# Kernel optimization log

Hardware: AMD Instinct MI355X
Metric: run time of the kernel (lower is better)

The kernel has to match this reference:

```python
import jax, jax.numpy as jnp
import numpy as np

N_QUBITS = 10
N_LAYERS = 4
OUTPUT = 16
BATCH = 4096
DIM = 2 ** N_QUBITS  # 1024, amplitude-embedding dimension


def setup_inputs() -> dict:
    key = jax.random.key(0)
    k1, k2, k3, k4 = jax.random.split(key, 4)
    X = jax.random.normal(k1, (BATCH, DIM), jnp.float32)
    weights = jax.random.normal(k2, (N_LAYERS, N_QUBITS, 3), jnp.float32)  # StronglyEntanglingLayers params
    W = jax.random.normal(k3, (OUTPUT, N_QUBITS), jnp.float32) / np.sqrt(N_QUBITS)
    b = jax.random.normal(k4, (OUTPUT,), jnp.float32) * 0.01
    return {"X": X, "weights": weights, "W": W, "b": b}


def _rot_matrix(phi, theta, omega):
    # PennyLane Rot(phi, theta, omega) = RZ(omega) @ RY(theta) @ RZ(phi)
    c = jnp.cos(theta / 2).astype(jnp.complex64)
    s = jnp.sin(theta / 2).astype(jnp.complex64)
    a = jnp.exp(-0.5j * (phi + omega)) * c
    bq = -jnp.exp(0.5j * (phi - omega)) * s
    cq = jnp.exp(-0.5j * (phi - omega)) * s
    d = jnp.exp(0.5j * (phi + omega)) * c
    return jnp.stack([jnp.stack([a, bq]), jnp.stack([cq, d])])  # (2,2) complex64


def _apply_1q(state, U, q, n):
    # wire 0 is the most-significant bit (PennyLane default.qubit convention)
    A, B = 2 ** q, 2 ** (n - q - 1)
    s = state.reshape(-1, A, 2, B)
    s = jnp.einsum('ij,bajc->baic', U, s)
    return s.reshape(-1, 2 ** n)


def _cnot(state, c, t, n):
    hi, lo = (c, t) if c < t else (t, c)
    s = state.reshape(-1, 2 ** hi, 2, 2 ** (lo - hi - 1), 2, 2 ** (n - lo - 1))
    if c < t:
        # control axis 2, target axis 4
        s0 = s[:, :, 0]                      # (B, H, M, 2, L)
        s1 = jnp.flip(s[:, :, 1], axis=3)    # flip target where control=1
        s = jnp.stack([s0, s1], axis=2)
    else:
        # control axis 4, target axis 2
        s0 = s[:, :, :, :, 0, :]             # (B, H, 2, M, L)
        s1 = jnp.flip(s[:, :, :, :, 1, :], axis=2)
        s = jnp.stack([s0, s1], axis=4)
    return s.reshape(-1, 2 ** n)


def _circuit(X, weights):
    n = N_QUBITS
    # AmplitudeEmbedding (pad_with=0.0; here input dim == 2**n so just normalize)
    nrm = jnp.linalg.norm(X, axis=-1, keepdims=True)
    state = (X / nrm).astype(jnp.complex64)  # (B, 2**n)
    for l in range(N_LAYERS):
        for q in range(n):
            U = _rot_matrix(weights[l, q, 0], weights[l, q, 1], weights[l, q, 2])
            state = _apply_1q(state, U, q, n)
        r = (l % (n - 1)) + 1  # StronglyEntanglingLayers default imprimitive range
        for q in range(n):
            state = _cnot(state, q, (q + r) % n, n)
    probs = state.real ** 2 + state.imag ** 2  # (B, 2**n)
    # <Z_i> = sum_s probs[s] * (1 - 2*bit_i(s)); wire 0 = MSB
    idx = np.arange(2 ** n)
    bits = (idx[:, None] >> np.arange(n - 1, -1, -1)[None, :]) & 1  # (2**n, n)
    signs = jnp.asarray(1 - 2 * bits, jnp.float32)
    return probs @ signs  # (B, n)


def reference(X, weights, W, b):
    z = _circuit(X, weights)          # (B, n_qubits)
    return z @ W.T + b                # Linear head; nn.Tanh is defined but unused in forward
```

## Files before the change

kernel.cpp:

```cpp
#include <hip/hip_runtime.h>
#include <stdint.h>

#define NQ 10
#define DIMQ 1024
#define BATCH 4096

typedef float f32x2 __attribute__((ext_vector_type(2)));

#if __has_builtin(__builtin_amdgcn_permlane16_swap)
#define HAS_PL16 1
#else
#define HAS_PL16 0
#endif

__host__ __device__ constexpr int cperm_c(int x, int r) {
  for (int q = 0; q < NQ; ++q) {
    const int c = 9 - q;
    int t = c - r; if (t < 0) t += NQ;
    x ^= ((x >> c) & 1) << t;
  }
  return x;
}
constexpr int amask(int q) {
  int a = 0;
  for (int b = 0; b < 6; ++b) a |= ((cperm_c(1 << b, 4) >> (9 - q)) & 1) << b;
  return a;
}
constexpr int mmask(int q) {
  int m = 0;
  for (int b = 0; b < 4; ++b) m |= ((cperm_c(1 << (6 + b), 4) >> (9 - q)) & 1) << b;
  return m;
}

__global__ __launch_bounds__(256) void prep_g(const float* __restrict__ wts,
                                              float* __restrict__ Gg) {
  const int idx = blockIdx.x * 256 + threadIdx.x;
  if (idx < 40) {
    float th = wts[idx * 3 + 1];
    ((float2*)Gg)[idx] = make_float2(cosf(0.5f * th), sinf(0.5f * th));
  }
  f32x2* D0 = (f32x2*)(Gg + 128);
  f32x2* E  = D0 + 1024;
  auto sphase = [&](int l, int i, int comp) {
    float s = 0.f;
    #pragma unroll
    for (int q = 0; q < 10; ++q) {
      float sg = ((i >> (9 - q)) & 1) ? 0.5f : -0.5f;
      s += sg * wts[(l * 10 + q) * 3 + comp];
    }
    return s;
  };
  float p0 = sphase(0, idx, 0);
  D0[idx] = (f32x2){cosf(p0), sinf(p0)};
  #pragma unroll
  for (int l = 0; l < 3; ++l) {
    float a = sphase(l, idx, 2) + sphase(l + 1, cperm_c(idx, l + 1), 0);
    E[l * 1024 + idx] = (f32x2){cosf(a), sinf(a)};
  }
}

template<int CTRL>
__device__ __forceinline__ float dpp1(float x) {
  return __int_as_float(
      __builtin_amdgcn_update_dpp(0, __float_as_int(x), CTRL, 0xF, 0xF, true));
}
template<int P>
__device__ __forceinline__ float shufl(float x) {
  if constexpr (P == 0)      return dpp1<0xB1>(x);
  else if constexpr (P == 1) return dpp1<0x4E>(x);
  else if constexpr (P == 2) return dpp1<0x141>(dpp1<0x1B>(x));
  else                       return dpp1<0x128>(x);
}
__device__ __forceinline__ float x16(float x, bool hi) {
#if HAS_PL16
  auto rr = __builtin_amdgcn_permlane16_swap(__float_as_uint(x),
                                             __float_as_uint(x), false, false);
  return __uint_as_float(hi ? rr[0] : rr[1]);
#else
  (void)hi;
  return __int_as_float(__builtin_amdgcn_ds_swizzle(__float_as_int(x), 0x401F));
#endif
}

__device__ __forceinline__ float red64(float v) {
  v += dpp1<0xB1>(v);
  v += dpp1<0x4E>(v);
  v += dpp1<0x141>(dpp1<0x1B>(v));
  v += dpp1<0x128>(v);
#if HAS_PL16
  { auto rr = __builtin_amdgcn_permlane16_swap(__float_as_uint(v),
                                               __float_as_uint(v), false, false);
    v = __uint_as_float(rr[0]) + __uint_as_float(rr[1]); }
#else
  v += __int_as_float(__builtin_amdgcn_ds_swizzle(__float_as_int(v), 0x401F));
#endif
  auto p = __builtin_amdgcn_permlane32_swap(__float_as_uint(v),
                                            __float_as_uint(v), false, false);
  return __uint_as_float(p[0]) + __uint_as_float(p[1]);
}

template<int MT>
__device__ __forceinline__ void ry_reg(f32x2 (&s)[16], float2 cs) {
  const float c = cs.x, sn = cs.y;
  #pragma unroll
  for (int e0 = 0; e0 < 16; ++e0) {
    if (e0 & MT) continue;
    const int e1 = e0 | MT;
    f32x2 x0 = s[e0], x1 = s[e1];
    s[e0] = c * x0 - sn * x1;
    s[e1] = sn * x0 + c * x1;
  }
}
template<int P>
__device__ __forceinline__ void ry_dpp(f32x2 (&s)[16], float2 cs, int lane) {
  const float c = cs.x;
  const float ss = ((lane >> P) & 1) ? cs.y : -cs.y;
  #pragma unroll
  for (int e = 0; e < 16; ++e) {
    f32x2 o;
    o.x = shufl<P>(s[e].x);
    o.y = shufl<P>(s[e].y);
    s[e] = c * s[e] + ss * o;
  }
}
__device__ __forceinline__ void ry16(f32x2 (&s)[16], float2 cs, int lane) {
  const bool H = (lane & 16) != 0;
  const float c = cs.x;
  const float ss = H ? cs.y : -cs.y;
  #pragma unroll
  for (int e = 0; e < 16; ++e) {
    f32x2 o;
    o.x = x16(s[e].x, H);
    o.y = x16(s[e].y, H);
    s[e] = c * s[e] + ss * o;
  }
}
__device__ __forceinline__ void ry5(f32x2 (&s)[16], float2 cs, int lane) {
  const int L = lane >> 5;
  const float c = cs.x;
  const float ss = L ? cs.y : -cs.y;
  #pragma unroll
  for (int e = 0; e < 16; ++e) {
    unsigned xr = __float_as_uint(s[e].x), xi = __float_as_uint(s[e].y);
    auto rr = __builtin_amdgcn_permlane32_swap(xr, xr, false, false);
    auto ri = __builtin_amdgcn_permlane32_swap(xi, xi, false, false);
    f32x2 o;
    o.x = __uint_as_float(L ? rr[0] : rr[1]);
    o.y = __uint_as_float(L ? ri[0] : ri[1]);
    s[e] = c * s[e] + ss * o;
  }
}

template<int R>
__device__ __forceinline__ void perm_state(f32x2 (&s)[16], f32x2* __restrict__ L,
                                           int lane) {
  constexpr int K0=cperm_c(1,R),  K1=cperm_c(2,R),  K2=cperm_c(4,R),
                K3=cperm_c(8,R),  K4=cperm_c(16,R), K5=cperm_c(32,R),
                C6=cperm_c(64,R), C7=cperm_c(128,R),
                C8=cperm_c(256,R),C9=cperm_c(512,R);
  const int yl = ((lane & 1)  ? K0 : 0) ^ ((lane & 2)  ? K1 : 0) ^
                 ((lane & 4)  ? K2 : 0) ^ ((lane & 8)  ? K3 : 0) ^
                 ((lane & 16) ? K4 : 0) ^ ((lane & 32) ? K5 : 0);
  #pragma unroll
  for (int e = 0; e < 16; ++e) {
    const int ye = ((e & 1) ? C6 : 0) ^ ((e & 2) ? C7 : 0) ^
                   ((e & 4) ? C8 : 0) ^ ((e & 8) ? C9 : 0);
    L[yl ^ ye] = s[e];
  }
  #pragma unroll
  for (int e = 0; e < 16; ++e) s[e] = L[(e << 6) | lane];
}

template<int LYR>
__device__ __forceinline__ void do_layer(f32x2 (&s)[16],
                                         const float2* __restrict__ ryc,
                                         const f32x2* __restrict__ Etab,
                                         f32x2* __restrict__ L, int lane) {
  f32x2 et[16];
  if constexpr (LYR < 3) {
    const f32x2* El = Etab + LYR * 1024;
    #pragma unroll
    for (int e = 0; e < 16; ++e) et[e] = El[(e << 6) | lane];
  }
  const float2* G = ryc + LYR * 10;
  ry_reg<8>(s, G[0]);
  ry_reg<4>(s, G[1]);
  ry_reg<2>(s, G[2]);
  ry_reg<1>(s, G[3]);
  ry5     (s, G[4], lane);
  ry16    (s, G[5], lane);
  ry_dpp<3>(s, G[6], lane);
  ry_dpp<2>(s, G[7], lane);
  ry_dpp<1>(s, G[8], lane);
  ry_dpp<0>(s, G[9], lane);
  if constexpr (LYR < 3) {
    #pragma unroll
    for (int e = 0; e < 16; ++e) {
      f32x2 t = et[e];
      f32x2 r;
      r.x = s[e].x * t.x - s[e].y * t.y;
      r.y = s[e].x * t.y + s[e].y * t.x;
      s[e] = r;
    }
    perm_state<LYR + 1>(s, L, lane);
  }
}

template<int M>
__device__ __forceinline__ void wht(float (&h)[16]) {
  #pragma unroll
  for (int e0 = 0; e0 < 16; ++e0) {
    if (e0 & M) continue;
    float u = h[e0], v = h[e0 | M];
    h[e0] = u + v;
    h[e0 | M] = u - v;
  }
}
template<int Q>
__device__ __forceinline__ float zfin(const float (&h)[16], int lane, float rn2) {
  constexpr int aq = amask(Q);
  constexpr int mq = mmask(Q);
  float t = h[mq];
  if constexpr (aq != 0) {
    int par = __builtin_popcount(lane & aq) & 1;
    t = par ? -t : t;
  }
  return red64(t) * rn2;
}

__global__ __launch_bounds__(256, 2) void vqc_sim(const float* __restrict__ X,
                                                  const float* __restrict__ Gg,
                                                  const float* __restrict__ W,
                                                  const float* __restrict__ bias,
                                                  float* __restrict__ out) {
  __shared__ f32x2 lds[4][DIMQ];
  const int lane = threadIdx.x & 63;
  const int w = threadIdx.x >> 6;
  const int row = blockIdx.x * 4 + w;
  f32x2* L = lds[w];
  const float2* ryc = (const float2*)Gg;
  const f32x2* D0   = (const f32x2*)(Gg + 128);
  const f32x2* Etab = D0 + 1024;

  f32x2 s[16];

  const float* xr = X + (size_t)row * DIMQ;
  float ss = 0.f;
  #pragma unroll
  for (int e = 0; e < 16; ++e) {
    float v = xr[(e << 6) | lane];
    ss += v * v;
    s[e] = v * D0[(e << 6) | lane];
  }
  const float rn2 = 1.0f / red64(ss);

  do_layer<0>(s, ryc, Etab, L, lane);
  do_layer<1>(s, ryc, Etab, L, lane);
  do_layer<2>(s, ryc, Etab, L, lane);
  do_layer<3>(s, ryc, Etab, L, lane);

  float h[16];
  #pragma unroll
  for (int e = 0; e < 16; ++e) h[e] = s[e].x * s[e].x + s[e].y * s[e].y;
  wht<1>(h); wht<2>(h); wht<4>(h); wht<8>(h);

  float z[10];
  z[0] = zfin<0>(h, lane, rn2);
  z[1] = zfin<1>(h, lane, rn2);
  z[2] = zfin<2>(h, lane, rn2);
  z[3] = zfin<3>(h, lane, rn2);
  z[4] = zfin<4>(h, lane, rn2);
  z[5] = zfin<5>(h, lane, rn2);
  z[6] = zfin<6>(h, lane, rn2);
  z[7] = zfin<7>(h, lane, rn2);
  z[8] = zfin<8>(h, lane, rn2);
  z[9] = zfin<9>(h, lane, rn2);

  if (lane < 16) {
    float acc = bias[lane];
    #pragma unroll
    for (int q = 0; q < 10; ++q) acc += z[q] * W[lane * 10 + q];
    out[(size_t)row * 16 + lane] = acc;
  }
}

extern "C" void kernel_launch(void* const* d_in, const int* in_sizes, int n_in,
                              void* d_out, int out_size, void* d_ws, size_t ws_size,
                              hipStream_t stream) {
  const float* X    = (const float*)d_in[0];
  const float* wts  = (const float*)d_in[1];
  const float* W    = (const float*)d_in[2];
  const float* bias = (const float*)d_in[3];
  float* out = (float*)d_out;
  float* Gg = (float*)d_ws;

  hipLaunchKernelGGL(prep_g,  dim3(4),         dim3(256), 0, stream, wts, Gg);
  hipLaunchKernelGGL(vqc_sim, dim3(BATCH / 4), dim3(256), 0, stream, X, Gg, W, bias, out);
}
```

Baseline: 99.42 us.

## Split each state vector across two wavefronts with LDS exchange for top qubit

Each batch row is now simulated by a 128-thread block of two wavefronts, each holding half the amplitudes (8 complex registers per lane instead of 16). The top-qubit rotation, which was a register-local butterfly, becomes an LDS exchange between the two wavefronts. Permutations and the final reduction now also need block-level barriers and a shared combine step. This halves register pressure and doubles the number of wavefronts per row to raise occupancy and latency hiding, at the cost of extra __syncthreads and LDS traffic per layer.

```diff
diff --git a/kernel.cpp b/kernel.cpp
--- a/kernel.cpp
+++ b/kernel.cpp
@@ -28,9 +28,10 @@
 }
 constexpr int mmask(int q) {
   int m = 0;
-  for (int b = 0; b < 4; ++b) m |= ((cperm_c(1 << (6 + b), 4) >> (9 - q)) & 1) << b;
+  for (int b = 0; b < 3; ++b) m |= ((cperm_c(1 << (6 + b), 4) >> (9 - q)) & 1) << b;
   return m;
 }
+constexpr int hmask(int q) { return (cperm_c(512, 4) >> (9 - q)) & 1; }
 
 __global__ __launch_bounds__(256) void prep_g(const float* __restrict__ wts,
                                               float* __restrict__ Gg) {
@@ -100,10 +101,10 @@
 }
 
 template<int MT>
-__device__ __forceinline__ void ry_reg(f32x2 (&s)[16], float2 cs) {
+__device__ __forceinline__ void ry_reg(f32x2 (&s)[8], float2 cs) {
   const float c = cs.x, sn = cs.y;
   #pragma unroll
-  for (int e0 = 0; e0 < 16; ++e0) {
+  for (int e0 = 0; e0 < 8; ++e0) {
     if (e0 & MT) continue;
     const int e1 = e0 | MT;
     f32x2 x0 = s[e0], x1 = s[e1];
@@ -112,35 +113,35 @@
   }
 }
 template<int P>
-__device__ __forceinline__ void ry_dpp(f32x2 (&s)[16], float2 cs, int lane) {
+__device__ __forceinline__ void ry_dpp(f32x2 (&s)[8], float2 cs, int lane) {
   const float c = cs.x;
   const float ss = ((lane >> P) & 1) ? cs.y : -cs.y;
   #pragma unroll
-  for (int e = 0; e < 16; ++e) {
+  for (int e = 0; e < 8; ++e) {
     f32x2 o;
     o.x = shufl<P>(s[e].x);
     o.y = shufl<P>(s[e].y);
     s[e] = c * s[e] + ss * o;
   }
 }
-__device__ __forceinline__ void ry16(f32x2 (&s)[16], float2 cs, int lane) {
+__device__ __forceinline__ void ry16(f32x2 (&s)[8], float2 cs, int lane) {
   const bool H = (lane & 16) != 0;
   const float c = cs.x;
   const float ss = H ? cs.y : -cs.y;
   #pragma unroll
-  for (int e = 0; e < 16; ++e) {
+  for (int e = 0; e < 8; ++e) {
     f32x2 o;
     o.x = x16(s[e].x, H);
     o.y = x16(s[e].y, H);
     s[e] = c * s[e] + ss * o;
   }
 }
-__device__ __forceinline__ void ry5(f32x2 (&s)[16], float2 cs, int lane) {
+__device__ __forceinline__ void ry5(f32x2 (&s)[8], float2 cs, int lane) {
   const int L = lane >> 5;
   const float c = cs.x;
   const float ss = L ? cs.y : -cs.y;
   #pragma unroll
-  for (int e = 0; e < 16; ++e) {
+  for (int e = 0; e < 8; ++e) {
     unsigned xr = __float_as_uint(s[e].x), xi = __float_as_uint(s[e].y);
     auto rr = __builtin_amdgcn_permlane32_swap(xr, xr, false, false);
     auto ri = __builtin_amdgcn_permlane32_swap(xi, xi, false, false);
@@ -151,39 +152,65 @@
   }
 }
 
+template<bool FIRST>
+__device__ __forceinline__ void ry_wave(f32x2 (&s)[8], float2 cs,
+                                        f32x2* __restrict__ buf,
+                                        int lane, int h, float& ss) {
+  f32x2* wp = buf + ((h << 9) | lane);
+  #pragma unroll
+  for (int e = 0; e < 8; ++e) wp[e << 6] = s[e];
+  if (FIRST && lane == 0) buf[1024 + h] = (f32x2){ss, 0.f};
+  __syncthreads();
+  const float c = cs.x;
+  const float sn = h ? cs.y : -cs.y;
+  const f32x2* rp = buf + (((h ^ 1) << 9) | lane);
+  #pragma unroll
+  for (int e = 0; e < 8; ++e) {
+    f32x2 o = rp[e << 6];
+    s[e] = c * s[e] + sn * o;
+  }
+  if (FIRST) ss += buf[1024 + (h ^ 1)].x;
+  __syncthreads();
+}
+
 template<int R>
-__device__ __forceinline__ void perm_state(f32x2 (&s)[16], f32x2* __restrict__ L,
-                                           int lane) {
+__device__ __forceinline__ void perm_state(f32x2 (&s)[8], f32x2* __restrict__ buf,
+                                           int lane, int h) {
   constexpr int K0=cperm_c(1,R),  K1=cperm_c(2,R),  K2=cperm_c(4,R),
                 K3=cperm_c(8,R),  K4=cperm_c(16,R), K5=cperm_c(32,R),
                 C6=cperm_c(64,R), C7=cperm_c(128,R),
                 C8=cperm_c(256,R),C9=cperm_c(512,R);
   const int yl = ((lane & 1)  ? K0 : 0) ^ ((lane & 2)  ? K1 : 0) ^
                  ((lane & 4)  ? K2 : 0) ^ ((lane & 8)  ? K3 : 0) ^
-                 ((lane & 16) ? K4 : 0) ^ ((lane & 32) ? K5 : 0);
-  #pragma unroll
-  for (int e = 0; e < 16; ++e) {
-    const int ye = ((e & 1) ? C6 : 0) ^ ((e & 2) ? C7 : 0) ^
-                   ((e & 4) ? C8 : 0) ^ ((e & 8) ? C9 : 0);
-    L[yl ^ ye] = s[e];
-  }
-  #pragma unroll
-  for (int e = 0; e < 16; ++e) s[e] = L[(e << 6) | lane];
+                 ((lane & 16) ? K4 : 0) ^ ((lane & 32) ? K5 : 0) ^
+                 (h ? C9 : 0);
+  #pragma unroll
+  for (int e = 0; e < 8; ++e) {
+    const int y = yl ^ (((e & 1) ? C6 : 0) ^ ((e & 2) ? C7 : 0) ^
+                        ((e & 4) ? C8 : 0));
+    buf[y] = s[e];
+  }
+  __syncthreads();
+  const f32x2* rp = buf + ((h << 9) | lane);
+  #pragma unroll
+  for (int e = 0; e < 8; ++e) s[e] = rp[e << 6];
+  __syncthreads();
 }
 
 template<int LYR>
-__device__ __forceinline__ void do_layer(f32x2 (&s)[16],
+__device__ __forceinline__ void do_layer(f32x2 (&s)[8],
                                          const float2* __restrict__ ryc,
                                          const f32x2* __restrict__ Etab,
-                                         f32x2* __restrict__ L, int lane) {
-  f32x2 et[16];
+                                         f32x2* __restrict__ buf,
+                                         int lane, int h, float& ss) {
+  f32x2 et[8];
   if constexpr (LYR < 3) {
-    const f32x2* El = Etab + LYR * 1024;
+    const f32x2* El = Etab + LYR * 1024 + (h << 9);
     #pragma unroll
-    for (int e = 0; e < 16; ++e) et[e] = El[(e << 6) | lane];
+    for (int e = 0; e < 8; ++e) et[e] = El[(e << 6) | lane];
   }
   const float2* G = ryc + LYR * 10;
-  ry_reg<8>(s, G[0]);
+  ry_wave<LYR == 0>(s, G[0], buf, lane, h, ss);
   ry_reg<4>(s, G[1]);
   ry_reg<2>(s, G[2]);
   ry_reg<1>(s, G[3]);
@@ -195,91 +222,96 @@
   ry_dpp<0>(s, G[9], lane);
   if constexpr (LYR < 3) {
     #pragma unroll
-    for (int e = 0; e < 16; ++e) {
+    for (int e = 0; e < 8; ++e) {
       f32x2 t = et[e];
       f32x2 r;
       r.x = s[e].x * t.x - s[e].y * t.y;
       r.y = s[e].x * t.y + s[e].y * t.x;
       s[e] = r;
     }
-    perm_state<LYR + 1>(s, L, lane);
+    perm_state<LYR + 1>(s, buf, lane, h);
   }
 }
 
 template<int M>
-__device__ __forceinline__ void wht(float (&h)[16]) {
-  #pragma unroll
-  for (int e0 = 0; e0 < 16; ++e0) {
+__device__ __forceinline__ void wht(float (&hh)[8]) {
+  #pragma unroll
+  for (int e0 = 0; e0 < 8; ++e0) {
     if (e0 & M) continue;
-    float u = h[e0], v = h[e0 | M];
-    h[e0] = u + v;
-    h[e0 | M] = u - v;
+    float u = hh[e0], v = hh[e0 | M];
+    hh[e0] = u + v;
+    hh[e0 | M] = u - v;
   }
 }
 template<int Q>
-__device__ __forceinline__ float zfin(const float (&h)[16], int lane, float rn2) {
+__device__ __forceinline__ float zfin(const float (&hh)[8], int lane, int h) {
   constexpr int aq = amask(Q);
   constexpr int mq = mmask(Q);
-  float t = h[mq];
-  if constexpr (aq != 0) {
-    int par = __builtin_popcount(lane & aq) & 1;
-    t = par ? -t : t;
-  }
-  return red64(t) * rn2;
-}
-
-__global__ __launch_bounds__(256, 2) void vqc_sim(const float* __restrict__ X,
+  constexpr int hq = hmask(Q);
+  float t = hh[mq];
+  int par = (__builtin_popcount(lane & aq) + (hq ? h : 0)) & 1;
+  t = par ? -t : t;
+  return red64(t);
+}
+
+__global__ __launch_bounds__(128, 4) void vqc_sim(const float* __restrict__ X,
                                                   const float* __restrict__ Gg,
                                                   const float* __restrict__ W,
                                                   const float* __restrict__ bias,
                                                   float* __restrict__ out) {
-  __shared__ f32x2 lds[4][DIMQ];
+  __shared__ f32x2 buf[1026];
+  __shared__ float zbuf[2][10];
   const int lane = threadIdx.x & 63;
-  const int w = threadIdx.x >> 6;
-  const int row = blockIdx.x * 4 + w;
-  f32x2* L = lds[w];
+  const int h = threadIdx.x >> 6;
+  const int row = blockIdx.x;
   const float2* ryc = (const float2*)Gg;
   const f32x2* D0   = (const f32x2*)(Gg + 128);
   const f32x2* Etab = D0 + 1024;
 
-  f32x2 s[16];
-
-  const float* xr = X + (size_t)row * DIMQ;
+  f32x2 s[8];
+
+  const float* xr = X + (size_t)row * DIMQ + (h << 9);
+  const f32x2* D0h = D0 + (h << 9);
   float ss = 0.f;
   #pragma unroll
-  for (int e = 0; e < 16; ++e) {
+  for (int e = 0; e < 8; ++e) {
     float v = xr[(e << 6) | lane];
     ss += v * v;
-    s[e] = v * D0[(e << 6) | lane];
-  }
-  const float rn2 = 1.0f / red64(ss);
-
-  do_layer<0>(s, ryc, Etab, L, lane);
-  do_layer<1>(s, ryc, Etab, L, lane);
-  do_layer<2>(s, ryc, Etab, L, lane);
-  do_layer<3>(s, ryc, Etab, L, lane);
-
-  float h[16];
-  #pragma unroll
-  for (int e = 0; e < 16; ++e) h[e] = s[e].x * s[e].x + s[e].y * s[e].y;
-  wht<1>(h); wht<2>(h); wht<4>(h); wht<8>(h);
+    s[e] = v * D0h[(e << 6) | lane];
+  }
+  ss = red64(ss);
+
+  do_layer<0>(s, ryc, Etab, buf, lane, h, ss);
+  do_layer<1>(s, ryc, Etab, buf, lane, h, ss);
+  do_layer<2>(s, ryc, Etab, buf, lane, h, ss);
+  do_layer<3>(s, ryc, Etab, buf, lane, h, ss);
+
+  const float rn2 = 1.0f / ss;
+
+  float hh[8];
+  #pragma unroll
+  for (int e = 0; e < 8; ++e) hh[e] = s[e].x * s[e].x + s[e].y * s[e].y;
+  wht<1>(hh); wht<2>(hh); wht<4>(hh);
 
   float z[10];
-  z[0] = zfin<0>(h, lane, rn2);
-  z[1] = zfin<1>(h, lane, rn2);
-  z[2] = zfin<2>(h, lane, rn2);
-  z[3] = zfin<3>(h, lane, rn2);
-  z[4] = zfin<4>(h, lane, rn2);
-  z[5] = zfin<5>(h, lane, rn2);
-  z[6] = zfin<6>(h, lane, rn2);
-  z[7] = zfin<7>(h, lane, rn2);
-  z[8] = zfin<8>(h, lane, rn2);
-  z[9] = zfin<9>(h, lane, rn2);
-
-  if (lane < 16) {
+  z[0] = zfin<0>(hh, lane, h);
+  z[1] = zfin<1>(hh, lane, h);
+  z[2] = zfin<2>(hh, lane, h);
+  z[3] = zfin<3>(hh, lane, h);
+  z[4] = zfin<4>(hh, lane, h);
+  z[5] = zfin<5>(hh, lane, h);
+  z[6] = zfin<6>(hh, lane, h);
+  z[7] = zfin<7>(hh, lane, h);
+  z[8] = zfin<8>(hh, lane, h);
+  z[9] = zfin<9>(hh, lane, h);
+
+  if (lane < 10) zbuf[h][lane] = z[lane];
+  __syncthreads();
+  if (h == 0 && lane < 16) {
     float acc = bias[lane];
     #pragma unroll
-    for (int q = 0; q < 10; ++q) acc += z[q] * W[lane * 10 + q];
+    for (int q = 0; q < 10; ++q)
+      acc += (zbuf[0][q] + zbuf[1][q]) * rn2 * W[lane * 10 + q];
     out[(size_t)row * 16 + lane] = acc;
   }
 }
@@ -294,6 +326,6 @@
   float* out = (float*)d_out;
   float* Gg = (float*)d_ws;
 
-  hipLaunchKernelGGL(prep_g,  dim3(4),         dim3(256), 0, stream, wts, Gg);
-  hipLaunchKernelGGL(vqc_sim, dim3(BATCH / 4), dim3(256), 0, stream, X, Gg, W, bias, out);
-}
+  hipLaunchKernelGGL(prep_g,  dim3(4),     dim3(256), 0, stream, wts, Gg);
+  hipLaunchKernelGGL(vqc_sim, dim3(BATCH), dim3(128), 0, stream, X, Gg, W, bias, out);
+}
```

Measured after the change: 104.3 us. 4.9% more time.
